# Kernel tuning notes

Hardware: AMD Instinct MI355X
Metric: run time of the kernel (lower is better)

The kernel has to match this reference:

```python
import jax, jax.numpy as jnp
import numpy as np


def setup_inputs() -> dict:
    key = jax.random.key(0)
    k1, k2, k3, k4, k5 = jax.random.split(key, 5)
    S, B, He, Hd, A = 2048, 32, 1024, 1024, 512
    dec_out = jax.random.normal(k1, (B, Hd), dtype=jnp.float32)
    enc_outs = jax.random.normal(k2, (S, B, He), dtype=jnp.float32)
    # parameter scales matching nn.Linear default init (~U(-1/sqrt(fan_in), ...))
    W_enc = jax.random.normal(k3, (A, He), dtype=jnp.float32) / np.sqrt(He)
    W_dec = jax.random.normal(k4, (A, Hd), dtype=jnp.float32) / np.sqrt(Hd)
    att_v = jax.random.normal(k5, (A,), dtype=jnp.float32) / np.sqrt(A)
    return {"dec_out": dec_out, "enc_outs": enc_outs, "W_enc": W_enc,
            "W_dec": W_dec, "att_v": att_v}


def reference(dec_out, enc_outs, W_enc, W_dec, att_v):
    # enc_att: (S, B, A) = enc_outs @ W_enc^T
    enc_att = jnp.einsum('sbh,ah->sba', enc_outs, W_enc)
    # dec_att: (B, A) = dec_out @ W_dec^T, tiled over seq_len
    dec_att = jnp.einsum('bh,ah->ba', dec_out, W_dec)
    # additive score: tanh(enc_att + dec_att) . att_v  -> (B, S)
    dec_enc_att = jnp.tanh(enc_att + dec_att[None, :, :])      # (S, B, A)
    scores = jnp.einsum('sba,a->bs', dec_enc_att, att_v)       # (B, S)
    weights = jax.nn.softmax(scores, axis=-1)                  # (B, S)
    # context: weighted sum of encoder outputs -> (B, He)
    context = jnp.einsum('bs,sbh->bh', weights, enc_outs)
    return context, weights
```

## Files before the change

kernel.cpp:

```cpp
#include <hip/hip_runtime.h>
#include <hip/hip_bf16.h>


typedef float f32x4 __attribute__((ext_vector_type(4)));
typedef __bf16 bf16x8 __attribute__((ext_vector_type(8)));

#define WS_DEC_OFF    0u
#define WS_WIMG_OFF   65536u
#define WS_SCORES_OFF (65536u + 1048576u)
#define WS_PART_OFF   (65536u + 1048576u + 262144u)

#define WAITLGKM0() asm volatile("s_waitcnt lgkmcnt(0)" ::: "memory")
#define SBAR()      asm volatile("s_barrier" ::: "memory")

__global__ void dec_att_kernel(const float* __restrict__ dec_out,
                               const float* __restrict__ W_dec,
                               float* __restrict__ out) {
  int gtid = blockIdx.x * blockDim.x + threadIdx.x;
  int w = gtid >> 6;
  int lane = gtid & 63;
  int b = w >> 9;
  int a = w & 511;
  const float4* dp = (const float4*)(dec_out + b * 1024);
  const float4* wp = (const float4*)(W_dec + a * 1024);
  float sum = 0.f;
#pragma unroll
  for (int i = 0; i < 4; ++i) {
    float4 x = dp[lane + i * 64];
    float4 y = wp[lane + i * 64];
    sum += x.x * y.x + x.y * y.y + x.z * y.z + x.w * y.w;
  }
#pragma unroll
  for (int m = 32; m; m >>= 1) sum += __shfl_xor(sum, m, 64);
  if (lane == 0) out[b * 512 + a] = sum;
}

__global__ void convert_wenc(const float* __restrict__ W, __bf16* __restrict__ out) {
  int idx = blockIdx.x * 256 + threadIdx.x;
  int kc = idx >> 14;
  int row = (idx >> 5) & 511;
  int j = idx & 31;
  out[idx] = (__bf16)W[row * 1024 + kc * 32 + j];
}

__global__ __launch_bounds__(256, 2) void scores_gemm(
    const float* __restrict__ enc,
    const __bf16* __restrict__ wimg,
    const float* __restrict__ dec_att,
    const float* __restrict__ attv,
    float* __restrict__ scores) {
  __shared__ __align__(16) char smem[8192];
  float (*part)[4] = (float(*)[4])smem;

  const int tid = threadIdx.x;
  const int lane = tid & 63;
  const int wc = tid >> 6;
  const int q = lane >> 4;
  const int c0 = lane & 15;
  const int bm = blockIdx.x;

  f32x4 acc[4][8];
#pragma unroll
  for (int i = 0; i < 4; ++i)
#pragma unroll
    for (int j = 0; j < 8; ++j) acc[i][j] = (f32x4){0.f, 0.f, 0.f, 0.f};

  const int srow = tid >> 2;
  const int sq = tid & 3;
  const float* asrc = enc + (size_t)(bm * 64 + srow) * 1024 + sq * 8;
  const int a_woff = srow * 64 + (((sq + (srow >> 1)) & 3) << 4);
  int a_roff[4];
#pragma unroll
  for (int mf = 0; mf < 4; ++mf) {
    const int row = mf * 16 + c0;
    a_roff[mf] = row * 64 + (((q + (row >> 1)) & 3) << 4);
  }

  const char* bptr = (const char*)wimg + (wc * 128 + c0) * 64 + q * 16;

  bf16x8 bcur[8], bnxt[8];

  {
    const float4* as4 = (const float4*)asrc;
    float4 x = as4[0], y = as4[1];
#pragma unroll
    for (int nf = 0; nf < 8; ++nf)
      bcur[nf] = *(const bf16x8*)(bptr + nf * 1024);
    bf16x8 v;
    v[0] = (__bf16)x.x; v[1] = (__bf16)x.y; v[2] = (__bf16)x.z; v[3] = (__bf16)x.w;
    v[4] = (__bf16)y.x; v[5] = (__bf16)y.y; v[6] = (__bf16)y.z; v[7] = (__bf16)y.w;
    *(bf16x8*)(smem + a_woff) = v;
  }
  __syncthreads();

  for (int t = 0; t < 32; ++t) {
    const int cur = t & 1;
    char* ab = smem + cur * 4096;
    float4 an0, an1;
    if (t < 31) {
      const float4* as4 = (const float4*)(asrc + (t + 1) * 32);
      an0 = as4[0]; an1 = as4[1];
      const char* bs = bptr + (size_t)(t + 1) * 32768;
#pragma unroll
      for (int nf = 0; nf < 8; ++nf)
        bnxt[nf] = *(const bf16x8*)(bs + nf * 1024);
    }
    bf16x8 af[4];
#pragma unroll
    for (int mf = 0; mf < 4; ++mf) af[mf] = *(const bf16x8*)(ab + a_roff[mf]);
    __builtin_amdgcn_s_setprio(1);
#pragma unroll
    for (int mf = 0; mf < 4; ++mf)
#pragma unroll
      for (int nf = 0; nf < 8; ++nf)
        acc[mf][nf] = __builtin_amdgcn_mfma_f32_16x16x32_bf16(af[mf], bcur[nf],
                                                              acc[mf][nf], 0, 0, 0);
    __builtin_amdgcn_s_setprio(0);
    if (t < 31) {
      bf16x8 v;
      v[0] = (__bf16)an0.x; v[1] = (__bf16)an0.y; v[2] = (__bf16)an0.z; v[3] = (__bf16)an0.w;
      v[4] = (__bf16)an1.x; v[5] = (__bf16)an1.y; v[6] = (__bf16)an1.z; v[7] = (__bf16)an1.w;
      *(bf16x8*)(smem + (cur ^ 1) * 4096 + a_woff) = v;
#pragma unroll
      for (int nf = 0; nf < 8; ++nf) bcur[nf] = bnxt[nf];
    }
    WAITLGKM0();
    SBAR();
  }

  float av[8];
#pragma unroll
  for (int nf = 0; nf < 8; ++nf) av[nf] = attv[wc * 128 + nf * 16 + c0];

#pragma unroll
  for (int mf = 0; mf < 4; ++mf) {
#pragma unroll
    for (int rg = 0; rg < 4; ++rg) {
      const int rl = mf * 16 + q * 4 + rg;
      const int b = rl & 31;
      const float* drow = dec_att + b * 512 + wc * 128 + c0;
      float sum = 0.f;
#pragma unroll
      for (int nf = 0; nf < 8; ++nf) {
        float x = acc[mf][nf][rg] + drow[nf * 16];
        float e = __expf(2.f * x);
        float t = 1.f - 2.f / (e + 1.f);
        sum += t * av[nf];
      }
      sum += __shfl_xor(sum, 1, 64);
      sum += __shfl_xor(sum, 2, 64);
      sum += __shfl_xor(sum, 4, 64);
      sum += __shfl_xor(sum, 8, 64);
      if (c0 == 0) part[rl][wc] = sum;
    }
  }
  __syncthreads();
  if (tid < 64) {
    float tot = part[tid][0] + part[tid][1] + part[tid][2] + part[tid][3];
    int r = bm * 64 + tid;
    scores[(r & 31) * 2048 + (r >> 5)] = tot;
  }
}

__global__ void softmax_kernel(const float* __restrict__ scores,
                               float* __restrict__ weights) {
  const int b = blockIdx.x;
  const int t = threadIdx.x;
  const float4* row = (const float4*)(scores + b * 2048);
  float4 v0 = row[t];
  float4 v1 = row[t + 256];
  float m = fmaxf(fmaxf(fmaxf(v0.x, v0.y), fmaxf(v0.z, v0.w)),
                  fmaxf(fmaxf(v1.x, v1.y), fmaxf(v1.z, v1.w)));
#pragma unroll
  for (int s = 32; s; s >>= 1) m = fmaxf(m, __shfl_xor(m, s, 64));
  __shared__ float redm[4], reds[4];
  if ((t & 63) == 0) redm[t >> 6] = m;
  __syncthreads();
  m = fmaxf(fmaxf(redm[0], redm[1]), fmaxf(redm[2], redm[3]));
  float4 e0, e1;
  e0.x = __expf(v0.x - m); e0.y = __expf(v0.y - m);
  e0.z = __expf(v0.z - m); e0.w = __expf(v0.w - m);
  e1.x = __expf(v1.x - m); e1.y = __expf(v1.y - m);
  e1.z = __expf(v1.z - m); e1.w = __expf(v1.w - m);
  float s8 = e0.x + e0.y + e0.z + e0.w + e1.x + e1.y + e1.z + e1.w;
#pragma unroll
  for (int s = 32; s; s >>= 1) s8 += __shfl_xor(s8, s, 64);
  if ((t & 63) == 0) reds[t >> 6] = s8;
  __syncthreads();
  float inv = 1.f / (reds[0] + reds[1] + reds[2] + reds[3]);
  e0.x *= inv; e0.y *= inv; e0.z *= inv; e0.w *= inv;
  e1.x *= inv; e1.y *= inv; e1.z *= inv; e1.w *= inv;
  float4* wrow = (float4*)(weights + b * 2048);
  wrow[t] = e0;
  wrow[t + 256] = e1;
}

__global__ void ctx_partial(const float* __restrict__ enc,
                            const float* __restrict__ weights,
                            float* __restrict__ part) {
  const int b = blockIdx.x & 31;
  const int sc = blockIdx.x >> 5;
  const int t = threadIdx.x;
  const float* wrow = weights + b * 2048 + sc * 128;
  const char* ebase = (const char*)(enc + ((size_t)(sc * 128) * 32 + b) * 1024) + t * 16;
  float4 acc = {0.f, 0.f, 0.f, 0.f};
#pragma unroll 4
  for (int i = 0; i < 128; ++i) {
    float4 e = *(const float4*)(ebase + (size_t)i * 131072);
    float ws = wrow[i];
    acc.x += ws * e.x; acc.y += ws * e.y; acc.z += ws * e.z; acc.w += ws * e.w;
  }
  *(float4*)(part + (size_t)(sc * 32 + b) * 1024 + t * 4) = acc;
}

__global__ void ctx_reduce(const float* __restrict__ part, float* __restrict__ ctx) {
  int idx = blockIdx.x * 256 + threadIdx.x;
  float s = 0.f;
#pragma unroll
  for (int c = 0; c < 16; ++c) s += part[c * 32768 + idx];
  ctx[idx] = s;
}

extern "C" void kernel_launch(void* const* d_in, const int* in_sizes, int n_in,
                              void* d_out, int out_size, void* d_ws, size_t ws_size,
                              hipStream_t stream) {
  const float* dec_out  = (const float*)d_in[0];
  const float* enc_outs = (const float*)d_in[1];
  const float* W_enc    = (const float*)d_in[2];
  const float* W_dec    = (const float*)d_in[3];
  const float* att_v    = (const float*)d_in[4];

  float* out = (float*)d_out;
  float* ctx = out;
  float* weights = out + 32768;

  char* ws = (char*)d_ws;
  float*  ws_dec    = (float*)(ws + WS_DEC_OFF);
  __bf16* ws_wimg   = (__bf16*)(ws + WS_WIMG_OFF);
  float*  ws_scores = (float*)(ws + WS_SCORES_OFF);
  float*  ws_part   = (float*)(ws + WS_PART_OFF);

  dec_att_kernel<<<4096, 256, 0, stream>>>(dec_out, W_dec, ws_dec);
  convert_wenc<<<2048, 256, 0, stream>>>(W_enc, ws_wimg);
  scores_gemm<<<1024, 256, 0, stream>>>(enc_outs, ws_wimg, ws_dec, att_v, ws_scores);
  softmax_kernel<<<32, 256, 0, stream>>>(ws_scores, weights);
  ctx_partial<<<512, 256, 0, stream>>>(enc_outs, weights, ws_part);
  ctx_reduce<<<128, 256, 0, stream>>>(ws_part, ctx);
}
```

Measured before the change: 161.8 us.

## Split scores GEMM into single-wave blocks loading A directly into registers

The scores GEMM moves from 256-thread blocks with a shared-memory A tile and barriers to 64-thread single-wave blocks. Each block covers 32 rows by 128 attention columns and loads fp32 encoder rows straight into registers with a two-stage register pipeline. The four column-block partial scores go to a workspace buffer, and the softmax kernel sums them. This removes LDS traffic and block-wide barriers, but each encoder tile is now read by four separate blocks instead of once, which raises global and L2 traffic.

```diff
diff --git a/kernel.cpp b/kernel.cpp
--- a/kernel.cpp
+++ b/kernel.cpp
@@ -7,11 +7,8 @@
 
 #define WS_DEC_OFF    0u
 #define WS_WIMG_OFF   65536u
-#define WS_SCORES_OFF (65536u + 1048576u)
-#define WS_PART_OFF   (65536u + 1048576u + 262144u)
-
-#define WAITLGKM0() asm volatile("s_waitcnt lgkmcnt(0)" ::: "memory")
-#define SBAR()      asm volatile("s_barrier" ::: "memory")
+#define WS_PART_OFF   (65536u + 1048576u)
+#define WS_SPART_OFF  WS_PART_OFF
 
 __global__ void dec_att_kernel(const float* __restrict__ dec_out,
                                const float* __restrict__ W_dec,
@@ -43,145 +40,142 @@
   out[idx] = (__bf16)W[row * 1024 + kc * 32 + j];
 }
 
-__global__ __launch_bounds__(256, 2) void scores_gemm(
+__device__ __forceinline__ bf16x8 cvt8(const float4& x, const float4& y) {
+  bf16x8 v;
+  v[0] = (__bf16)x.x; v[1] = (__bf16)x.y; v[2] = (__bf16)x.z; v[3] = (__bf16)x.w;
+  v[4] = (__bf16)y.x; v[5] = (__bf16)y.y; v[6] = (__bf16)y.z; v[7] = (__bf16)y.w;
+  return v;
+}
+
+__device__ __forceinline__ void gstep(
+    int t, const char* aptr, const char* bptr,
+    float4& u00, float4& u01, float4& u10, float4& u11,
+    float4& l00, float4& l01, float4& l10, float4& l11,
+    bf16x8* bu, bf16x8* bl,
+    f32x4 acc[2][8]) {
+  bf16x8 af0 = cvt8(u00, u01);
+  bf16x8 af1 = cvt8(u10, u11);
+  const int tn = (t + 1 > 31) ? 31 : t + 1;
+  {
+    const char* ap = aptr + tn * 128;
+    l00 = *(const float4*)(ap);
+    l01 = *(const float4*)(ap + 16);
+    l10 = *(const float4*)(ap + 16 * 4096);
+    l11 = *(const float4*)(ap + 16 * 4096 + 16);
+    const char* bp = bptr + (size_t)tn * 32768;
+#pragma unroll
+    for (int nf = 0; nf < 8; ++nf)
+      bl[nf] = *(const bf16x8*)(bp + nf * 1024);
+  }
+  __builtin_amdgcn_s_setprio(1);
+#pragma unroll
+  for (int nf = 0; nf < 8; ++nf) {
+    acc[0][nf] = __builtin_amdgcn_mfma_f32_16x16x32_bf16(af0, bu[nf], acc[0][nf], 0, 0, 0);
+    acc[1][nf] = __builtin_amdgcn_mfma_f32_16x16x32_bf16(af1, bu[nf], acc[1][nf], 0, 0, 0);
+  }
+  __builtin_amdgcn_s_setprio(0);
+}
+
+__global__ __launch_bounds__(64, 2) void scores_gemm(
     const float* __restrict__ enc,
     const __bf16* __restrict__ wimg,
     const float* __restrict__ dec_att,
     const float* __restrict__ attv,
-    float* __restrict__ scores) {
-  __shared__ __align__(16) char smem[8192];
-  float (*part)[4] = (float(*)[4])smem;
-
-  const int tid = threadIdx.x;
-  const int lane = tid & 63;
-  const int wc = tid >> 6;
+    float* __restrict__ spart) {
+  const int lane = threadIdx.x;
   const int q = lane >> 4;
   const int c0 = lane & 15;
-  const int bm = blockIdx.x;
-
-  f32x4 acc[4][8];
-#pragma unroll
-  for (int i = 0; i < 4; ++i)
+  const int d = blockIdx.x;
+  const int m = ((d >> 5) << 3) | (d & 7);
+  const int nb = (d >> 3) & 3;
+
+  f32x4 acc[2][8];
+#pragma unroll
+  for (int i = 0; i < 2; ++i)
 #pragma unroll
     for (int j = 0; j < 8; ++j) acc[i][j] = (f32x4){0.f, 0.f, 0.f, 0.f};
 
-  const int srow = tid >> 2;
-  const int sq = tid & 3;
-  const float* asrc = enc + (size_t)(bm * 64 + srow) * 1024 + sq * 8;
-  const int a_woff = srow * 64 + (((sq + (srow >> 1)) & 3) << 4);
-  int a_roff[4];
-#pragma unroll
-  for (int mf = 0; mf < 4; ++mf) {
-    const int row = mf * 16 + c0;
-    a_roff[mf] = row * 64 + (((q + (row >> 1)) & 3) << 4);
-  }
-
-  const char* bptr = (const char*)wimg + (wc * 128 + c0) * 64 + q * 16;
-
-  bf16x8 bcur[8], bnxt[8];
+  const char* aptr = (const char*)enc + ((size_t)(m * 32 + c0)) * 4096 + q * 32;
+  const char* bptr = (const char*)wimg + (nb * 128 + c0) * 64 + q * 16;
+
+  float4 aP00, aP01, aP10, aP11, aQ00, aQ01, aQ10, aQ11;
+  bf16x8 bP[8], bQ[8];
 
   {
-    const float4* as4 = (const float4*)asrc;
-    float4 x = as4[0], y = as4[1];
+    aP00 = *(const float4*)(aptr);
+    aP01 = *(const float4*)(aptr + 16);
+    aP10 = *(const float4*)(aptr + 16 * 4096);
+    aP11 = *(const float4*)(aptr + 16 * 4096 + 16);
 #pragma unroll
     for (int nf = 0; nf < 8; ++nf)
-      bcur[nf] = *(const bf16x8*)(bptr + nf * 1024);
-    bf16x8 v;
-    v[0] = (__bf16)x.x; v[1] = (__bf16)x.y; v[2] = (__bf16)x.z; v[3] = (__bf16)x.w;
-    v[4] = (__bf16)y.x; v[5] = (__bf16)y.y; v[6] = (__bf16)y.z; v[7] = (__bf16)y.w;
-    *(bf16x8*)(smem + a_woff) = v;
-  }
-  __syncthreads();
-
-  for (int t = 0; t < 32; ++t) {
-    const int cur = t & 1;
-    char* ab = smem + cur * 4096;
-    float4 an0, an1;
-    if (t < 31) {
-      const float4* as4 = (const float4*)(asrc + (t + 1) * 32);
-      an0 = as4[0]; an1 = as4[1];
-      const char* bs = bptr + (size_t)(t + 1) * 32768;
-#pragma unroll
-      for (int nf = 0; nf < 8; ++nf)
-        bnxt[nf] = *(const bf16x8*)(bs + nf * 1024);
-    }
-    bf16x8 af[4];
-#pragma unroll
-    for (int mf = 0; mf < 4; ++mf) af[mf] = *(const bf16x8*)(ab + a_roff[mf]);
-    __builtin_amdgcn_s_setprio(1);
-#pragma unroll
-    for (int mf = 0; mf < 4; ++mf)
-#pragma unroll
-      for (int nf = 0; nf < 8; ++nf)
-        acc[mf][nf] = __builtin_amdgcn_mfma_f32_16x16x32_bf16(af[mf], bcur[nf],
-                                                              acc[mf][nf], 0, 0, 0);
-    __builtin_amdgcn_s_setprio(0);
-    if (t < 31) {
-      bf16x8 v;
-      v[0] = (__bf16)an0.x; v[1] = (__bf16)an0.y; v[2] = (__bf16)an0.z; v[3] = (__bf16)an0.w;
-      v[4] = (__bf16)an1.x; v[5] = (__bf16)an1.y; v[6] = (__bf16)an1.z; v[7] = (__bf16)an1.w;
-      *(bf16x8*)(smem + (cur ^ 1) * 4096 + a_woff) = v;
-#pragma unroll
-      for (int nf = 0; nf < 8; ++nf) bcur[nf] = bnxt[nf];
-    }
-    WAITLGKM0();
-    SBAR();
+      bP[nf] = *(const bf16x8*)(bptr + nf * 1024);
+  }
+
+#pragma unroll 1
+  for (int tt = 0; tt < 16; ++tt) {
+    gstep(2 * tt,     aptr, bptr, aP00, aP01, aP10, aP11,
+          aQ00, aQ01, aQ10, aQ11, bP, bQ, acc);
+    gstep(2 * tt + 1, aptr, bptr, aQ00, aQ01, aQ10, aQ11,
+          aP00, aP01, aP10, aP11, bQ, bP, acc);
   }
 
   float av[8];
 #pragma unroll
-  for (int nf = 0; nf < 8; ++nf) av[nf] = attv[wc * 128 + nf * 16 + c0];
-
-#pragma unroll
-  for (int mf = 0; mf < 4; ++mf) {
+  for (int nf = 0; nf < 8; ++nf) av[nf] = attv[nb * 128 + nf * 16 + c0];
+
+#pragma unroll
+  for (int mf = 0; mf < 2; ++mf) {
 #pragma unroll
     for (int rg = 0; rg < 4; ++rg) {
       const int rl = mf * 16 + q * 4 + rg;
-      const int b = rl & 31;
-      const float* drow = dec_att + b * 512 + wc * 128 + c0;
+      const float* drow = dec_att + rl * 512 + nb * 128 + c0;
       float sum = 0.f;
 #pragma unroll
       for (int nf = 0; nf < 8; ++nf) {
         float x = acc[mf][nf][rg] + drow[nf * 16];
         float e = __expf(2.f * x);
-        float t = 1.f - 2.f / (e + 1.f);
-        sum += t * av[nf];
+        float th = 1.f - 2.f / (e + 1.f);
+        sum += th * av[nf];
       }
       sum += __shfl_xor(sum, 1, 64);
       sum += __shfl_xor(sum, 2, 64);
       sum += __shfl_xor(sum, 4, 64);
       sum += __shfl_xor(sum, 8, 64);
-      if (c0 == 0) part[rl][wc] = sum;
+      if (c0 == 0) spart[nb * 65536 + rl * 2048 + m] = sum;
     }
   }
-  __syncthreads();
-  if (tid < 64) {
-    float tot = part[tid][0] + part[tid][1] + part[tid][2] + part[tid][3];
-    int r = bm * 64 + tid;
-    scores[(r & 31) * 2048 + (r >> 5)] = tot;
-  }
-}
-
-__global__ void softmax_kernel(const float* __restrict__ scores,
+}
+
+__global__ void softmax_kernel(const float* __restrict__ spart,
                                float* __restrict__ weights) {
   const int b = blockIdx.x;
   const int t = threadIdx.x;
-  const float4* row = (const float4*)(scores + b * 2048);
-  float4 v0 = row[t];
-  float4 v1 = row[t + 256];
-  float m = fmaxf(fmaxf(fmaxf(v0.x, v0.y), fmaxf(v0.z, v0.w)),
-                  fmaxf(fmaxf(v1.x, v1.y), fmaxf(v1.z, v1.w)));
-#pragma unroll
-  for (int s = 32; s; s >>= 1) m = fmaxf(m, __shfl_xor(m, s, 64));
+  const float4* p0 = (const float4*)(spart + b * 2048);
+  const float4* p1 = (const float4*)(spart + 65536 + b * 2048);
+  const float4* p2 = (const float4*)(spart + 131072 + b * 2048);
+  const float4* p3 = (const float4*)(spart + 196608 + b * 2048);
+  float4 v0, v1;
+  {
+    float4 a0 = p0[t], a1 = p1[t], a2 = p2[t], a3 = p3[t];
+    v0.x = a0.x + a1.x + a2.x + a3.x; v0.y = a0.y + a1.y + a2.y + a3.y;
+    v0.z = a0.z + a1.z + a2.z + a3.z; v0.w = a0.w + a1.w + a2.w + a3.w;
+    a0 = p0[t + 256]; a1 = p1[t + 256]; a2 = p2[t + 256]; a3 = p3[t + 256];
+    v1.x = a0.x + a1.x + a2.x + a3.x; v1.y = a0.y + a1.y + a2.y + a3.y;
+    v1.z = a0.z + a1.z + a2.z + a3.z; v1.w = a0.w + a1.w + a2.w + a3.w;
+  }
+  float mx = fmaxf(fmaxf(fmaxf(v0.x, v0.y), fmaxf(v0.z, v0.w)),
+                   fmaxf(fmaxf(v1.x, v1.y), fmaxf(v1.z, v1.w)));
+#pragma unroll
+  for (int s = 32; s; s >>= 1) mx = fmaxf(mx, __shfl_xor(mx, s, 64));
   __shared__ float redm[4], reds[4];
-  if ((t & 63) == 0) redm[t >> 6] = m;
+  if ((t & 63) == 0) redm[t >> 6] = mx;
   __syncthreads();
-  m = fmaxf(fmaxf(redm[0], redm[1]), fmaxf(redm[2], redm[3]));
+  mx = fmaxf(fmaxf(redm[0], redm[1]), fmaxf(redm[2], redm[3]));
   float4 e0, e1;
-  e0.x = __expf(v0.x - m); e0.y = __expf(v0.y - m);
-  e0.z = __expf(v0.z - m); e0.w = __expf(v0.w - m);
-  e1.x = __expf(v1.x - m); e1.y = __expf(v1.y - m);
-  e1.z = __expf(v1.z - m); e1.w = __expf(v1.w - m);
+  e0.x = __expf(v0.x - mx); e0.y = __expf(v0.y - mx);
+  e0.z = __expf(v0.z - mx); e0.w = __expf(v0.w - mx);
+  e1.x = __expf(v1.x - mx); e1.y = __expf(v1.y - mx);
+  e1.z = __expf(v1.z - mx); e1.w = __expf(v1.w - mx);
   float s8 = e0.x + e0.y + e0.z + e0.w + e1.x + e1.y + e1.z + e1.w;
 #pragma unroll
   for (int s = 32; s; s >>= 1) s8 += __shfl_xor(s8, s, 64);
@@ -237,13 +231,13 @@
   char* ws = (char*)d_ws;
   float*  ws_dec    = (float*)(ws + WS_DEC_OFF);
   __bf16* ws_wimg   = (__bf16*)(ws + WS_WIMG_OFF);
-  float*  ws_scores = (float*)(ws + WS_SCORES_OFF);
+  float*  ws_spart  = (float*)(ws + WS_SPART_OFF);
   float*  ws_part   = (float*)(ws + WS_PART_OFF);
 
   dec_att_kernel<<<4096, 256, 0, stream>>>(dec_out, W_dec, ws_dec);
   convert_wenc<<<2048, 256, 0, stream>>>(W_enc, ws_wimg);
-  scores_gemm<<<1024, 256, 0, stream>>>(enc_outs, ws_wimg, ws_dec, att_v, ws_scores);
-  softmax_kernel<<<32, 256, 0, stream>>>(ws_scores, weights);
+  scores_gemm<<<8192, 64, 0, stream>>>(enc_outs, ws_wimg, ws_dec, att_v, ws_spart);
+  softmax_kernel<<<32, 256, 0, stream>>>(ws_spart, weights);
   ctx_partial<<<512, 256, 0, stream>>>(enc_outs, weights, ws_part);
   ctx_reduce<<<128, 256, 0, stream>>>(ws_part, ctx);
 }
```

After: 302.8 us. +87.1%, slower.
